# Optimization experiments

Hardware: AMD Instinct MI355X
Metric: run time of the kernel (lower is better)

## Reference

```python
import jax, jax.numpy as jnp
import numpy as np

N = 100000
E = 1600000
EPS = 1e-16
NEG_SLOPE = 0.2


def setup_inputs() -> dict:
    key = jax.random.key(0)
    ks = jax.random.split(key, 10)
    F_in, C = 512, 40
    H1, D1 = 8, 8
    return {
        "x": jax.random.normal(ks[0], (N, F_in), jnp.float32),
        "edge_index": jax.random.randint(ks[1], (2, E), 0, N, jnp.int64),
        "W1": jax.random.normal(ks[2], (F_in, H1 * D1), jnp.float32) * 0.05,
        "att_src1": jax.random.normal(ks[3], (H1, D1), jnp.float32) * 0.1,
        "att_dst1": jax.random.normal(ks[4], (H1, D1), jnp.float32) * 0.1,
        "b1": jnp.zeros((H1 * D1,), jnp.float32),
        "W2": jax.random.normal(ks[5], (H1 * D1, C), jnp.float32) * 0.05,
        "att_src2": jax.random.normal(ks[6], (1, C), jnp.float32) * 0.1,
        "att_dst2": jax.random.normal(ks[7], (1, C), jnp.float32) * 0.1,
        "b2": jnp.zeros((C,), jnp.float32),
    }


def gat_conv(x, W, att_src, att_dst, bias, src, dst, heads, out_dim, concat):
    # Linear transform per head: [N, H, D]
    h = (x @ W).reshape(N, heads, out_dim)
    # Per-node attention logits: [N, H]
    a_src = jnp.einsum("nhd,hd->nh", h, att_src)
    a_dst = jnp.einsum("nhd,hd->nh", h, att_dst)
    # Per-edge logits (edge j->i: src=j, softmax grouped by dst=i)
    e = a_src[src] + a_dst[dst]                      # [E', H]
    e = jax.nn.leaky_relu(e, NEG_SLOPE)
    # Segment softmax over destination nodes (numerically stable)
    m = jax.ops.segment_max(e, dst, num_segments=N)  # [N, H]
    e = jnp.exp(e - m[dst])
    s = jax.ops.segment_sum(e, dst, num_segments=N)  # [N, H]
    alpha = e / (s[dst] + EPS)                       # [E', H]
    # Weighted message aggregation (scatter-add)
    msg = h[src] * alpha[:, :, None]                 # [E', H, D]
    out = jax.ops.segment_sum(msg, dst, num_segments=N)  # [N, H, D]
    out = out.reshape(N, heads * out_dim) if concat else out.mean(axis=1)
    return out + bias


def reference(x, edge_index, W1, att_src1, att_dst1, b1, W2, att_src2, att_dst2, b2):
    # PyG GATConv default: add self-loops
    loops = jnp.arange(N, dtype=edge_index.dtype)
    src = jnp.concatenate([edge_index[0], loops])
    dst = jnp.concatenate([edge_index[1], loops])
    h = gat_conv(x, W1, att_src1, att_dst1, b1, src, dst, heads=8, out_dim=8, concat=True)
    h = jax.nn.elu(h)
    out = gat_conv(h, W2, att_src2, att_dst2, b2, src, dst, heads=1, out_dim=40, concat=False)
    return jax.nn.log_softmax(out, axis=1)
```

## Files before the change

kernel.cpp:

```cpp
#include <hip/hip_runtime.h>
#include <cstdint>

#define N_NODES 100000
#define N_EDGES 1600000
#define ETOT    1700000
#define FIN     512
#define HD1     64
#define C2      40
#define NEG_SLOPE 0.2f
#define GEMM1_NB 782
#define ESL      2174
#define SCAN_NB2 98

typedef __attribute__((ext_vector_type(8))) short bf16x8;
typedef __attribute__((ext_vector_type(4))) float f32x4;

__device__ __forceinline__ float lrelu(float v) { return v > 0.f ? v : NEG_SLOPE * v; }

__device__ __forceinline__ unsigned short f2bf(float f) {
    uint32_t u = __float_as_uint(f);
    u += 0x7FFF + ((u >> 16) & 1);
    return (unsigned short)(u >> 16);
}
__device__ __forceinline__ float bf2f(unsigned short u) {
    return __uint_as_float(((uint32_t)u) << 16);
}

__global__ void k_prep(const float* __restrict__ W1, const float* __restrict__ a_s,
                       const float* __restrict__ a_d,
                       const float* __restrict__ W2, const float* __restrict__ att_s2,
                       const float* __restrict__ att_d2,
                       unsigned short* __restrict__ W1t, unsigned short* __restrict__ W2t,
                       int* __restrict__ deg, unsigned int* __restrict__ flags) {
    int i = blockIdx.x * 256 + threadIdx.x;
    if (i < N_NODES) deg[i] = 0;
    if (i < 128) flags[i] = 0u;
    if (i < 80 * 512) {
        int n = i >> 9, k = i & 511;
        float v;
        if (n < 64) {
            v = W1[k * HD1 + n];
        } else if (n < 72) {
            int h = n - 64; v = 0.f;
#pragma unroll
            for (int d = 0; d < 8; d++) v += W1[k * HD1 + h * 8 + d] * a_s[h * 8 + d];
        } else {
            int h = n - 72; v = 0.f;
#pragma unroll
            for (int d = 0; d < 8; d++) v += W1[k * HD1 + h * 8 + d] * a_d[h * 8 + d];
        }
        W1t[n * FIN + k] = f2bf(v);
    } else if (i < 80 * 512 + 48 * 64) {
        int j = i - 80 * 512;
        int n = j >> 6, k = j & 63;
        float v = 0.f;
        if (n < C2) {
            v = W2[k * C2 + n];
        } else if (n == C2) {
            for (int c = 0; c < C2; c++) v += W2[k * C2 + c] * att_s2[c];
        } else if (n == C2 + 1) {
            for (int c = 0; c < C2; c++) v += W2[k * C2 + c] * att_d2[c];
        }
        W2t[n * 64 + k] = f2bf(v);
    }
}

__global__ __launch_bounds__(256) void k_g1deg(const float* __restrict__ x,
                                               const unsigned short* __restrict__ W1t,
                                               unsigned short* __restrict__ h1b,
                                               float* __restrict__ as1,
                                               float* __restrict__ ad1,
                                               const int* __restrict__ ei,
                                               int* __restrict__ deg,
                                               int* __restrict__ ord) {
    __shared__ unsigned short As[128 * 72];
    const int t   = threadIdx.x;
    const int bid = blockIdx.x;
    const int e0 = bid * ESL;
    const int e1 = (e0 + ESL < ETOT) ? e0 + ESL : ETOT;
    const bool atomFirst = (bid & 1) == 0;

    if (atomFirst) {
        for (int e = e0 + t; e < e1; e += 256) {
            int dst = (e < N_EDGES) ? ei[N_EDGES + e] : e - N_EDGES;
            ord[e] = atomicAdd(&deg[dst], 1);
        }
    }

    const int lane = t & 63, wv = t >> 6;
    const int quad = lane >> 4, l16 = lane & 15;
    const int row0 = bid * 128;

    f32x4 acc[2][5];
#pragma unroll
    for (int mi = 0; mi < 2; mi++)
#pragma unroll
        for (int ni = 0; ni < 5; ni++) acc[mi][ni] = (f32x4){0.f, 0.f, 0.f, 0.f};

    float4 rx[8];
#pragma unroll
    for (int i = 0; i < 8; i++) {
        int ff = t + i * 256;
        int r = ff >> 4, c4 = ff & 15;
        int row = row0 + r;
        rx[i] = (row < N_NODES) ? *(const float4*)&x[(size_t)row * FIN + c4 * 4]
                                : make_float4(0.f, 0.f, 0.f, 0.f);
    }

    for (int c = 0; c < 8; c++) {
#pragma unroll
        for (int i = 0; i < 8; i++) {
            int ff = t + i * 256;
            int r = ff >> 4, c4 = ff & 15;
            ushort4 s4;
            s4.x = f2bf(rx[i].x); s4.y = f2bf(rx[i].y);
            s4.z = f2bf(rx[i].z); s4.w = f2bf(rx[i].w);
            *(ushort4*)&As[r * 72 + c4 * 4] = s4;
        }
        __syncthreads();
        if (c < 7) {
            int kb = (c + 1) * 64;
#pragma unroll
            for (int i = 0; i < 8; i++) {
                int ff = t + i * 256;
                int r = ff >> 4, c4 = ff & 15;
                int row = row0 + r;
                rx[i] = (row < N_NODES) ? *(const float4*)&x[(size_t)row * FIN + kb + c4 * 4]
                                        : make_float4(0.f, 0.f, 0.f, 0.f);
            }
        }
        int kb = c * 64;
#pragma unroll
        for (int ks = 0; ks < 2; ks++) {
            bf16x8 af[2], bfv[5];
#pragma unroll
            for (int mi = 0; mi < 2; mi++) {
                int lr = wv * 32 + mi * 16 + l16;
                af[mi] = *(const bf16x8*)&As[lr * 72 + ks * 32 + quad * 8];
            }
#pragma unroll
            for (int ni = 0; ni < 5; ni++) {
                int n = ni * 16 + l16;
                bfv[ni] = *(const bf16x8*)&W1t[n * FIN + kb + ks * 32 + quad * 8];
            }
#pragma unroll
            for (int mi = 0; mi < 2; mi++)
#pragma unroll
                for (int ni = 0; ni < 5; ni++)
                    acc[mi][ni] = __builtin_amdgcn_mfma_f32_16x16x32_bf16(
                        af[mi], bfv[ni], acc[mi][ni], 0, 0, 0);
        }
        __syncthreads();
    }
#pragma unroll
    for (int mi = 0; mi < 2; mi++)
#pragma unroll
        for (int ni = 0; ni < 5; ni++)
#pragma unroll
            for (int r = 0; r < 4; r++) {
                int row = row0 + wv * 32 + mi * 16 + quad * 4 + r;
                if (row >= N_NODES) continue;
                int col = ni * 16 + l16;
                float v = acc[mi][ni][r];
                if (col < 64)       h1b[(size_t)row * 64 + col] = f2bf(v);
                else if (col < 72)  as1[row * 8 + (col - 64)] = v;
                else                ad1[row * 8 + (col - 72)] = v;
            }

    if (!atomFirst) {
        for (int e = e0 + t; e < e1; e += 256) {
            int dst = (e < N_EDGES) ? ei[N_EDGES + e] : e - N_EDGES;
            ord[e] = atomicAdd(&deg[dst], 1);
        }
    }
}

__global__ __launch_bounds__(1024) void k_scan_lb(const int* __restrict__ deg,
                                                  int* __restrict__ row_ptr,
                                                  int* __restrict__ aggr,
                                                  int* __restrict__ incl,
                                                  unsigned int* __restrict__ flags) {
    __shared__ int sh[1024];
    __shared__ int shbase;
    const int t = threadIdx.x, b = blockIdx.x;
    const int i = b * 1024 + t;
    int v = (i < N_NODES) ? deg[i] : 0;
    sh[t] = v;
    __syncthreads();
    for (int off = 1; off < 1024; off <<= 1) {
        int u = (t >= off) ? sh[t - off] : 0;
        __syncthreads();
        sh[t] += u;
        __syncthreads();
    }
    if (t == 0) {
        int total = sh[1023];
        int run = 0;
        if (b == 0) {
            __hip_atomic_store(&incl[0], total, __ATOMIC_RELEASE, __HIP_MEMORY_SCOPE_AGENT);
            __hip_atomic_store(&flags[0], 2u, __ATOMIC_RELEASE, __HIP_MEMORY_SCOPE_AGENT);
        } else {
            __hip_atomic_store(&aggr[b], total, __ATOMIC_RELEASE, __HIP_MEMORY_SCOPE_AGENT);
            __hip_atomic_store(&flags[b], 1u, __ATOMIC_RELEASE, __HIP_MEMORY_SCOPE_AGENT);
            int p = b - 1;
            while (true) {
                unsigned int f = __hip_atomic_load(&flags[p], __ATOMIC_ACQUIRE,
                                                   __HIP_MEMORY_SCOPE_AGENT);
                if (f == 2u) {
                    run += __hip_atomic_load(&incl[p], __ATOMIC_ACQUIRE,
                                             __HIP_MEMORY_SCOPE_AGENT);
                    break;
                } else if (f == 1u) {
                    run += __hip_atomic_load(&aggr[p], __ATOMIC_ACQUIRE,
                                             __HIP_MEMORY_SCOPE_AGENT);
                    --p;
                }
            }
            __hip_atomic_store(&incl[b], run + total, __ATOMIC_RELEASE,
                               __HIP_MEMORY_SCOPE_AGENT);
            __hip_atomic_store(&flags[b], 2u, __ATOMIC_RELEASE, __HIP_MEMORY_SCOPE_AGENT);
        }
        shbase = run;
        if (b == 0) row_ptr[N_NODES] = ETOT;
    }
    __syncthreads();
    int base = shbase;
    if (i < N_NODES) row_ptr[i] = base + sh[t] - v;
}

__global__ void k_scatter(const int* __restrict__ ei, const int* __restrict__ row_ptr,
                          const int* __restrict__ ord, int* __restrict__ csr_src) {
    int e = blockIdx.x * 256 + threadIdx.x;
    if (e >= ETOT) return;
    int src, dst;
    if (e < N_EDGES) { src = ei[e]; dst = ei[N_EDGES + e]; }
    else             { src = dst = e - N_EDGES; }
    csr_src[row_ptr[dst] + ord[e]] = src;
}

__global__ __launch_bounds__(256) void k_agg1(
    const unsigned short* __restrict__ h1b,
    const float* __restrict__ as1, const float* __restrict__ ad1,
    const int* __restrict__ row_ptr, const int* __restrict__ csr_src,
    const float* __restrict__ b1, unsigned short* __restrict__ hb) {
    int t = threadIdx.x, wv = t >> 6, lane = t & 63;
    int dst = blockIdx.x * 4 + wv;
    if (dst >= N_NODES) return;
    int g = lane >> 3, i8 = lane & 7;
    int s0 = row_ptr[dst], s1e = row_ptr[dst + 1];
    float adh = ad1[dst * 8 + i8];
    float den = 0.f;
    float facc[8];
#pragma unroll
    for (int d = 0; d < 8; d++) facc[d] = 0.f;

    for (int base = s0; base < s1e; base += 64) {
        int idx = base + lane;
        int sl = (idx < s1e) ? csr_src[idx] : 0;
        int cnt = min(64, s1e - base);
        for (int j = 0; j < cnt; j += 16) {
            int sA = __shfl(sl, j + g);
            int sB = __shfl(sl, j + 8 + g);
            bool vA = (j + g) < cnt, vB = (j + 8 + g) < cnt;
            bf16x8 rA = *(const bf16x8*)&h1b[(size_t)sA * 64 + i8 * 8];
            bf16x8 rB = *(const bf16x8*)&h1b[(size_t)sB * 64 + i8 * 8];
            float aA = as1[sA * 8 + i8];
            float aB = as1[sB * 8 + i8];
            float wA = vA ? __expf(lrelu(aA + adh)) : 0.f;
            float wB = vB ? __expf(lrelu(aB + adh)) : 0.f;
            den += wA + wB;
#pragma unroll
            for (int d = 0; d < 8; d++)
                facc[d] += wA * bf2f((unsigned short)rA[d]) +
                           wB * bf2f((unsigned short)rB[d]);
        }
    }
#pragma unroll
    for (int o = 8; o <= 32; o <<= 1) {
        den += __shfl_xor(den, o, 64);
#pragma unroll
        for (int d = 0; d < 8; d++) facc[d] += __shfl_xor(facc[d], o, 64);
    }
    float rden = 1.f / (den + 1e-16f);
    float4 b1lo = *(const float4*)&b1[i8 * 8];
    float4 b1hi = *(const float4*)&b1[i8 * 8 + 4];
    float bb[8] = {b1lo.x, b1lo.y, b1lo.z, b1lo.w, b1hi.x, b1hi.y, b1hi.z, b1hi.w};
    bf16x8 pk;
#pragma unroll
    for (int d = 0; d < 8; d++) {
        float hv = facc[d] * rden + bb[d];
        hv = hv > 0.f ? hv : expm1f(hv);
        pk[d] = (short)f2bf(hv);
    }
    if (g == 0) *(bf16x8*)&hb[(size_t)dst * 64 + i8 * 8] = pk;
}

__global__ __launch_bounds__(256) void k_gemm2(const unsigned short* __restrict__ hb,
                                               const unsigned short* __restrict__ W2t,
                                               unsigned short* __restrict__ h2b,
                                               float* __restrict__ as2,
                                               float* __restrict__ ad2) {
    const int t = threadIdx.x;
    const int lane = t & 63, wv = t >> 6;
    const int quad = lane >> 4, l16 = lane & 15;
    const int row0 = blockIdx.x * 128;

    f32x4 acc[2][3];
#pragma unroll
    for (int mi = 0; mi < 2; mi++)
#pragma unroll
        for (int ni = 0; ni < 3; ni++) acc[mi][ni] = (f32x4){0.f, 0.f, 0.f, 0.f};

    bf16x8 bfrag[2][3];
#pragma unroll
    for (int ks = 0; ks < 2; ks++)
#pragma unroll
        for (int ni = 0; ni < 3; ni++)
            bfrag[ks][ni] = *(const bf16x8*)&W2t[(ni * 16 + l16) * 64 + ks * 32 + quad * 8];

#pragma unroll
    for (int mi = 0; mi < 2; mi++) {
        int row = row0 + wv * 32 + mi * 16 + l16;
        int rowc = row < N_NODES ? row : N_NODES - 1;
#pragma unroll
        for (int ks = 0; ks < 2; ks++) {
            bf16x8 af = *(const bf16x8*)&hb[(size_t)rowc * 64 + ks * 32 + quad * 8];
#pragma unroll
            for (int ni = 0; ni < 3; ni++)
                acc[mi][ni] = __builtin_amdgcn_mfma_f32_16x16x32_bf16(
                    af, bfrag[ks][ni], acc[mi][ni], 0, 0, 0);
        }
    }
#pragma unroll
    for (int mi = 0; mi < 2; mi++)
#pragma unroll
        for (int ni = 0; ni < 3; ni++)
#pragma unroll
            for (int r = 0; r < 4; r++) {
                int row = row0 + wv * 32 + mi * 16 + quad * 4 + r;
                if (row >= N_NODES) continue;
                int col = ni * 16 + l16;
                float v = acc[mi][ni][r];
                if (col < C2)            h2b[(size_t)row * C2 + col] = f2bf(v);
                else if (col == C2)      as2[row] = v;
                else if (col == C2 + 1)  ad2[row] = v;
            }
}

__global__ __launch_bounds__(256) void k_agg2(
    const unsigned short* __restrict__ h2b,
    const float* __restrict__ as2, const float* __restrict__ ad2,
    const int* __restrict__ row_ptr, const int* __restrict__ csr_src,
    const float* __restrict__ b2, float* __restrict__ out) {
    int t = threadIdx.x, wv = t >> 6, lane = t & 63;
    int dst = blockIdx.x * 4 + wv;
    if (dst >= N_NODES) return;
    int g = lane >> 3, i8 = lane & 7;
    bool act = i8 < 5;
    int off = act ? i8 * 8 : 0;
    int s0 = row_ptr[dst], s1e = row_ptr[dst + 1];
    float ad = ad2[dst];
    float denp = 0.f;
    float facc[8];
#pragma unroll
    for (int d = 0; d < 8; d++) facc[d] = 0.f;

    for (int base = s0; base < s1e; base += 64) {
        int idx = base + lane;
        int sl = (idx < s1e) ? csr_src[idx] : 0;
        int cnt = min(64, s1e - base);
        for (int j = 0; j < cnt; j += 16) {
            int sA = __shfl(sl, j + g);
            int sB = __shfl(sl, j + 8 + g);
            bool vA = (j + g) < cnt, vB = (j + 8 + g) < cnt;
            bf16x8 rA = *(const bf16x8*)&h2b[(size_t)sA * C2 + off];
            bf16x8 rB = *(const bf16x8*)&h2b[(size_t)sB * C2 + off];
            float aA = as2[sA];
            float aB = as2[sB];
            float wfA = vA ? __expf(lrelu(aA + ad)) : 0.f;
            float wfB = vB ? __expf(lrelu(aB + ad)) : 0.f;
            if (i8 == 0) denp += wfA + wfB;
            float wA = act ? wfA : 0.f;
            float wB = act ? wfB : 0.f;
#pragma unroll
            for (int d = 0; d < 8; d++)
                facc[d] += wA * bf2f((unsigned short)rA[d]) +
                           wB * bf2f((unsigned short)rB[d]);
        }
    }
#pragma unroll
    for (int o = 8; o <= 32; o <<= 1)
#pragma unroll
        for (int d = 0; d < 8; d++) facc[d] += __shfl_xor(facc[d], o, 64);
    float den = denp;
#pragma unroll
    for (int o = 32; o >= 1; o >>= 1) den += __shfl_xor(den, o, 64);
    float rden = 1.f / (den + 1e-16f);

    float vch[8];
    float mx = -1e30f;
#pragma unroll
    for (int d = 0; d < 8; d++) {
        vch[d] = act ? facc[d] * rden + b2[off + d] : -1e30f;
        mx = fmaxf(mx, vch[d]);
    }
#pragma unroll
    for (int o = 1; o <= 4; o <<= 1) mx = fmaxf(mx, __shfl_xor(mx, o, 64));
    float es = 0.f;
#pragma unroll
    for (int d = 0; d < 8; d++) es += act ? __expf(vch[d] - mx) : 0.f;
#pragma unroll
    for (int o = 1; o <= 4; o <<= 1) es += __shfl_xor(es, o, 64);
    float lg = logf(es);
    if (g == 0 && act) {
        float4 o0 = {vch[0] - mx - lg, vch[1] - mx - lg, vch[2] - mx - lg, vch[3] - mx - lg};
        float4 o1 = {vch[4] - mx - lg, vch[5] - mx - lg, vch[6] - mx - lg, vch[7] - mx - lg};
        *(float4*)&out[(size_t)dst * C2 + i8 * 8]     = o0;
        *(float4*)&out[(size_t)dst * C2 + i8 * 8 + 4] = o1;
    }
}

extern "C" void kernel_launch(void* const* d_in, const int* in_sizes, int n_in,
                              void* d_out, int out_size, void* d_ws, size_t ws_size,
                              hipStream_t stream) {
    const float* x     = (const float*)d_in[0];
    const int*   ei    = (const int*)d_in[1];
    const float* W1    = (const float*)d_in[2];
    const float* at_s1 = (const float*)d_in[3];
    const float* at_d1 = (const float*)d_in[4];
    const float* b1    = (const float*)d_in[5];
    const float* W2    = (const float*)d_in[6];
    const float* at_s2 = (const float*)d_in[7];
    const float* at_d2 = (const float*)d_in[8];
    const float* b2    = (const float*)d_in[9];
    float* out = (float*)d_out;
    float* ws  = (float*)d_ws;

    unsigned short* h1b = (unsigned short*)ws;
    float* as1 = ws + 3200000;
    float* ad1 = ws + 4000000;
    unsigned short* hb  = (unsigned short*)(ws + 4800000);
    unsigned short* h2b = (unsigned short*)(ws + 8000000);
    float* as2 = ws + 10000000;
    float* ad2 = ws + 10100000;
    unsigned short* W1t = (unsigned short*)(ws + 10200000);
    unsigned short* W2t = (unsigned short*)(ws + 10250000);
    int* row_ptr = (int*)(ws + 10300000);
    int* deg     = (int*)(ws + 10410000);
    int* csr_src = (int*)(ws + 10630000);
    int* aggrA   = (int*)(ws + 12340000);
    int* inclA   = (int*)(ws + 12350000);
    unsigned int* flags = (unsigned int*)(ws + 12360000);
    int* ord     = (int*)(ws + 13000000);

    k_prep<<<391, 256, 0, stream>>>(W1, at_s1, at_d1, W2, at_s2, at_d2, W1t, W2t, deg, flags);
    k_g1deg<<<GEMM1_NB, 256, 0, stream>>>(x, W1t, h1b, as1, ad1, ei, deg, ord);
    k_scan_lb<<<SCAN_NB2, 1024, 0, stream>>>(deg, row_ptr, aggrA, inclA, flags);
    k_scatter<<<(ETOT + 255) / 256, 256, 0, stream>>>(ei, row_ptr, ord, csr_src);
    k_agg1<<<(N_NODES + 3) / 4, 256, 0, stream>>>(h1b, as1, ad1, row_ptr, csr_src, b1, hb);
    k_gemm2<<<(N_NODES + 127) / 128, 256, 0, stream>>>(hb, W2t, h2b, as2, ad2);
    k_agg2<<<(N_NODES + 3) / 4, 256, 0, stream>>>(h2b, as2, ad2, row_ptr, csr_src, b2, out);
}
```

Baseline: 562.4 us.

## Halve GEMM1 row tile, batch degree atomics and CSR scatter four per thread

The fused GEMM1+degree kernel now uses 64-row tiles (one 16-row MFMA strip per wave) with twice as many blocks, and always runs its edge-degree atomics after the GEMM. Those atomics are batched four per thread so loads and atomics can overlap. The scatter kernel likewise handles four edges per thread, issuing the independent loads before the stores. The aim is more parallelism for the GEMM and more memory-level parallelism in the atomic and scatter phases. The cost is that the W1 tile is reloaded by twice as many blocks and the previous alternating atomic/GEMM ordering is lost.

New measurement: 569.4 us. Within noise of the previous version (+1.2%).

```diff
diff --git a/kernel.cpp b/kernel.cpp
--- a/kernel.cpp
+++ b/kernel.cpp
@@ -8,8 +8,8 @@
 #define HD1     64
 #define C2      40
 #define NEG_SLOPE 0.2f
-#define GEMM1_NB 782
-#define ESL      2174
+#define GEMM1_NB 1563
+#define ESL      1088
 #define SCAN_NB2 98
 
 typedef __attribute__((ext_vector_type(8))) short bf16x8;
@@ -73,33 +73,20 @@
                                                const int* __restrict__ ei,
                                                int* __restrict__ deg,
                                                int* __restrict__ ord) {
-    __shared__ unsigned short As[128 * 72];
+    __shared__ unsigned short As[64 * 72];
     const int t   = threadIdx.x;
     const int bid = blockIdx.x;
-    const int e0 = bid * ESL;
-    const int e1 = (e0 + ESL < ETOT) ? e0 + ESL : ETOT;
-    const bool atomFirst = (bid & 1) == 0;
-
-    if (atomFirst) {
-        for (int e = e0 + t; e < e1; e += 256) {
-            int dst = (e < N_EDGES) ? ei[N_EDGES + e] : e - N_EDGES;
-            ord[e] = atomicAdd(&deg[dst], 1);
-        }
-    }
-
     const int lane = t & 63, wv = t >> 6;
     const int quad = lane >> 4, l16 = lane & 15;
-    const int row0 = bid * 128;
-
-    f32x4 acc[2][5];
-#pragma unroll
-    for (int mi = 0; mi < 2; mi++)
-#pragma unroll
-        for (int ni = 0; ni < 5; ni++) acc[mi][ni] = (f32x4){0.f, 0.f, 0.f, 0.f};
-
-    float4 rx[8];
-#pragma unroll
-    for (int i = 0; i < 8; i++) {
+    const int row0 = bid * 64;
+
+    f32x4 acc[5];
+#pragma unroll
+    for (int ni = 0; ni < 5; ni++) acc[ni] = (f32x4){0.f, 0.f, 0.f, 0.f};
+
+    float4 rx[4];
+#pragma unroll
+    for (int i = 0; i < 4; i++) {
         int ff = t + i * 256;
         int r = ff >> 4, c4 = ff & 15;
         int row = row0 + r;
@@ -109,7 +96,7 @@
 
     for (int c = 0; c < 8; c++) {
 #pragma unroll
-        for (int i = 0; i < 8; i++) {
+        for (int i = 0; i < 4; i++) {
             int ff = t + i * 256;
             int r = ff >> 4, c4 = ff & 15;
             ushort4 s4;
@@ -121,7 +108,7 @@
         if (c < 7) {
             int kb = (c + 1) * 64;
 #pragma unroll
-            for (int i = 0; i < 8; i++) {
+            for (int i = 0; i < 4; i++) {
                 int ff = t + i * 256;
                 int r = ff >> 4, c4 = ff & 15;
                 int row = row0 + r;
@@ -132,46 +119,49 @@
         int kb = c * 64;
 #pragma unroll
         for (int ks = 0; ks < 2; ks++) {
-            bf16x8 af[2], bfv[5];
-#pragma unroll
-            for (int mi = 0; mi < 2; mi++) {
-                int lr = wv * 32 + mi * 16 + l16;
-                af[mi] = *(const bf16x8*)&As[lr * 72 + ks * 32 + quad * 8];
-            }
+            bf16x8 af, bfv[5];
+            af = *(const bf16x8*)&As[(wv * 16 + l16) * 72 + ks * 32 + quad * 8];
 #pragma unroll
             for (int ni = 0; ni < 5; ni++) {
                 int n = ni * 16 + l16;
                 bfv[ni] = *(const bf16x8*)&W1t[n * FIN + kb + ks * 32 + quad * 8];
             }
 #pragma unroll
-            for (int mi = 0; mi < 2; mi++)
-#pragma unroll
-                for (int ni = 0; ni < 5; ni++)
-                    acc[mi][ni] = __builtin_amdgcn_mfma_f32_16x16x32_bf16(
-                        af[mi], bfv[ni], acc[mi][ni], 0, 0, 0);
+            for (int ni = 0; ni < 5; ni++)
+                acc[ni] = __builtin_amdgcn_mfma_f32_16x16x32_bf16(af, bfv[ni], acc[ni], 0, 0, 0);
         }
         __syncthreads();
     }
 #pragma unroll
-    for (int mi = 0; mi < 2; mi++)
-#pragma unroll
-        for (int ni = 0; ni < 5; ni++)
-#pragma unroll
-            for (int r = 0; r < 4; r++) {
-                int row = row0 + wv * 32 + mi * 16 + quad * 4 + r;
-                if (row >= N_NODES) continue;
-                int col = ni * 16 + l16;
-                float v = acc[mi][ni][r];
-                if (col < 64)       h1b[(size_t)row * 64 + col] = f2bf(v);
-                else if (col < 72)  as1[row * 8 + (col - 64)] = v;
-                else                ad1[row * 8 + (col - 72)] = v;
-            }
-
-    if (!atomFirst) {
-        for (int e = e0 + t; e < e1; e += 256) {
-            int dst = (e < N_EDGES) ? ei[N_EDGES + e] : e - N_EDGES;
-            ord[e] = atomicAdd(&deg[dst], 1);
-        }
+    for (int ni = 0; ni < 5; ni++)
+#pragma unroll
+        for (int r = 0; r < 4; r++) {
+            int row = row0 + wv * 16 + quad * 4 + r;
+            if (row >= N_NODES) continue;
+            int col = ni * 16 + l16;
+            float v = acc[ni][r];
+            if (col < 64)       h1b[(size_t)row * 64 + col] = f2bf(v);
+            else if (col < 72)  as1[row * 8 + (col - 64)] = v;
+            else                ad1[row * 8 + (col - 72)] = v;
+        }
+
+    const int e0 = bid * ESL;
+    const int e1 = (e0 + ESL < ETOT) ? e0 + ESL : ETOT;
+    for (int eb = e0; eb < e1; eb += 1024) {
+        int ee[4], dd[4], rr[4];
+        bool vv[4];
+#pragma unroll
+        for (int u = 0; u < 4; u++) {
+            ee[u] = eb + u * 256 + t;
+            vv[u] = ee[u] < e1;
+            dd[u] = vv[u] ? ((ee[u] < N_EDGES) ? ei[N_EDGES + ee[u]] : ee[u] - N_EDGES) : 0;
+        }
+#pragma unroll
+        for (int u = 0; u < 4; u++)
+            if (vv[u]) rr[u] = atomicAdd(&deg[dd[u]], 1);
+#pragma unroll
+        for (int u = 0; u < 4; u++)
+            if (vv[u]) ord[ee[u]] = rr[u];
     }
 }
 
@@ -230,12 +220,23 @@
 
 __global__ void k_scatter(const int* __restrict__ ei, const int* __restrict__ row_ptr,
                           const int* __restrict__ ord, int* __restrict__ csr_src) {
-    int e = blockIdx.x * 256 + threadIdx.x;
-    if (e >= ETOT) return;
-    int src, dst;
-    if (e < N_EDGES) { src = ei[e]; dst = ei[N_EDGES + e]; }
-    else             { src = dst = e - N_EDGES; }
-    csr_src[row_ptr[dst] + ord[e]] = src;
+    int t = threadIdx.x;
+    int eb = blockIdx.x * 1024;
+    int ee[4], src[4], pos[4];
+    bool vv[4];
+#pragma unroll
+    for (int u = 0; u < 4; u++) {
+        ee[u] = eb + u * 256 + t;
+        vv[u] = ee[u] < ETOT;
+        int e = vv[u] ? ee[u] : 0;
+        int dst;
+        if (e < N_EDGES) { src[u] = ei[e]; dst = ei[N_EDGES + e]; }
+        else             { src[u] = dst = e - N_EDGES; }
+        pos[u] = vv[u] ? row_ptr[dst] : 0;
+    }
+#pragma unroll
+    for (int u = 0; u < 4; u++)
+        if (vv[u]) csr_src[pos[u] + ord[ee[u]]] = src[u];
 }
 
 __global__ __launch_bounds__(256) void k_agg1(
@@ -456,7 +457,7 @@
     k_prep<<<391, 256, 0, stream>>>(W1, at_s1, at_d1, W2, at_s2, at_d2, W1t, W2t, deg, flags);
     k_g1deg<<<GEMM1_NB, 256, 0, stream>>>(x, W1t, h1b, as1, ad1, ei, deg, ord);
     k_scan_lb<<<SCAN_NB2, 1024, 0, stream>>>(deg, row_ptr, aggrA, inclA, flags);
-    k_scatter<<<(ETOT + 255) / 256, 256, 0, stream>>>(ei, row_ptr, ord, csr_src);
+    k_scatter<<<(ETOT + 1023) / 1024, 256, 0, stream>>>(ei, row_ptr, ord, csr_src);
     k_agg1<<<(N_NODES + 3) / 4, 256, 0, stream>>>(h1b, as1, ad1, row_ptr, csr_src, b1, hb);
     k_gemm2<<<(N_NODES + 127) / 128, 256, 0, stream>>>(hb, W2t, h2b, as2, ad2);
     k_agg2<<<(N_NODES + 3) / 4, 256, 0, stream>>>(h2b, as2, ad2, row_ptr, csr_src, b2, out);
```
